# Optimization experiments

Measured on AMD Instinct MI355X. Metric: run time of the kernel, lower is better.

Reference implementation:

```python
import jax, jax.numpy as jnp
import numpy as np

# Sizes
N, E = 100000, 3200000
F_NODE, F_EDGE, LD, HID, L = 4, 4, 6, 16, 8
ALPHA = 1.0
EPS = 1e-6


def setup_inputs() -> dict:
    key = jax.random.key(0)
    ks = jax.random.split(key, 8)
    x = jax.random.normal(ks[0], (N, F_NODE), jnp.float32)
    fixed_mask = jax.random.uniform(ks[1], (N,)) < 0.1
    x = x.at[:, -1].set(jnp.where(fixed_mask, jnp.abs(x[:, -1]) + 1.0, 0.0))
    # positive edge attributes (pipe resistance etc.)
    edge_attr = jax.random.uniform(ks[2], (E, F_EDGE), jnp.float32) * 0.9 + 0.1
    edge_index = jax.random.randint(ks[3], (2, E), 0, N, dtype=jnp.int64)
    d_in = 2 * LD + 2 * F_NODE + F_EDGE  # 24: [x_src, x_dst, attr_src, attr_dst, edge_attr]
    s = 0.1
    W1 = jax.random.normal(ks[4], (L, d_in, HID), jnp.float32) * s
    b1 = jnp.zeros((L, HID), jnp.float32)
    W2 = jax.random.normal(ks[5], (L, HID, LD), jnp.float32) * s
    b2 = jnp.zeros((L, LD), jnp.float32)
    Wf = jax.random.normal(ks[6], (LD, 1), jnp.float32) * s
    bf = jnp.zeros((1,), jnp.float32)
    return {"x": x, "edge_attr": edge_attr, "edge_index": edge_index,
            "W1": W1, "b1": b1, "W2": W2, "b2": b2, "Wf": Wf, "bf": bf}


def reference(x, edge_attr, edge_index, W1, b1, W2, b2, Wf, bf):
    src, dst = edge_index[0], edge_index[1]
    # in-degree for mean aggregation
    deg = jax.ops.segment_sum(jnp.ones((E,), jnp.float32), dst, num_segments=N)
    deg = jnp.maximum(deg, 1.0)
    X = jnp.zeros((N, LD), jnp.float32)
    na_src, na_dst = x[src], x[dst]  # static node-attr gathers reused each layer
    for l in range(L):  # num_convs GNNSConv layers
        m_in = jnp.concatenate([X[src], X[dst], na_src, na_dst, edge_attr], axis=-1)  # [E,24]
        h = jax.nn.relu(m_in @ W1[l] + b1[l])         # per-edge MLP hidden [E,16]
        m = h @ W2[l] + b2[l]                          # per-edge message [E,6]
        agg = jax.ops.segment_sum(m, dst, num_segments=N) / deg[:, None]  # mean aggr
        X = (1.0 - ALPHA) * X + ALPHA * agg            # latent update (alpha_update_x)
        X = jax.nn.relu(X)
    P = jax.nn.relu(X @ Wf + bf)                       # [N,1]
    fixed = x[:, -1]
    P_ = jnp.where(fixed != 0, fixed, P.reshape(-1))   # keep known pressures
    # BalanceConv: gas-network flow from squared-pressure drop, k = edge resistance
    dp2 = P_[src] ** 2 - P_[dst] ** 2
    k = edge_attr[:, 0]
    flows = jnp.sign(dp2) * jnp.sqrt(jnp.abs(dp2) / k + EPS)  # [E]
    inj = x[:, 0]  # nodal injection/demand
    balance = (jax.ops.segment_sum(flows, dst, num_segments=N)
               - jax.ops.segment_sum(flows, src, num_segments=N) + inj)
    imbalance = jnp.sqrt(jnp.sum(balance ** 2))
    return P, flows, jnp.stack([imbalance])
```

## Files before the change

kernel.cpp:

```cpp
#include <hip/hip_runtime.h>
#include <math.h>

#define N_NODES 100000
#define N_EDGES 3200000
#define F_NODE 4
#define F_EDGE 4
#define LD 6
#define HID 16
#define NLAYER 8
#define EPSF 1e-6f

#define NPB 64
#define NBK 1563
#define NBIN 196
#define G1 1000
#define CH (N_EDGES / G1)
#define EPT ((CH + 255) / 256)
#define SPLIT 4
#define NSB (NBIN * SPLIT)

__device__ __forceinline__ unsigned f2bf(float a, float b) {
    unsigned ua = __float_as_uint(a);
    ua = (ua + 0x7fffu + ((ua >> 16) & 1u)) >> 16;
    unsigned ub = __float_as_uint(b);
    ub = (ub + 0x7fffu + ((ub >> 16) & 1u)) & 0xffff0000u;
    return ua | ub;
}
__device__ __forceinline__ float bflo(unsigned u) { return __uint_as_float(u << 16); }
__device__ __forceinline__ float bfhi(unsigned u) { return __uint_as_float(u & 0xffff0000u); }

__global__ __launch_bounds__(256) void hist_kernel(const int* __restrict__ ei,
                                                   int* __restrict__ ghd,
                                                   int* __restrict__ ghs) {
    __shared__ int hd[NBIN];
    __shared__ int hs[NBIN];
    int t = threadIdx.x, blk = blockIdx.x;
    for (int i = t; i < NBIN; i += 256) { hd[i] = 0; hs[i] = 0; }
    __syncthreads();
    int beg = blk * CH, end = beg + CH;
    for (int e = beg + t; e < end; e += 256) {
        atomicAdd(&hs[ei[e] >> 9], 1);
        atomicAdd(&hd[ei[N_EDGES + e] >> 9], 1);
    }
    __syncthreads();
    for (int i = t; i < NBIN; i += 256) {
        ghd[(size_t)i * G1 + blk] = hd[i];
        ghs[(size_t)i * G1 + blk] = hs[i];
    }
}

__global__ __launch_bounds__(256) void scanb_kernel(int* __restrict__ ghd, int* __restrict__ ghs,
                                                    int* __restrict__ totd, int* __restrict__ tots) {
    __shared__ int part[256];
    int b = blockIdx.x, t = threadIdx.x;
#pragma unroll
    for (int a = 0; a < 2; a++) {
        int* g = a ? ghs : ghd;
        int vals[4];
        int sum = 0;
#pragma unroll
        for (int k = 0; k < 4; k++) {
            int idx = t * 4 + k;
            vals[k] = (idx < G1) ? g[(size_t)b * G1 + idx] : 0;
            sum += vals[k];
        }
        part[t] = sum;
        __syncthreads();
        for (int off = 1; off < 256; off <<= 1) {
            int v = (t >= off) ? part[t - off] : 0;
            __syncthreads();
            part[t] += v;
            __syncthreads();
        }
        int excl = part[t] - sum;
#pragma unroll
        for (int k = 0; k < 4; k++) {
            int idx = t * 4 + k;
            if (idx < G1) g[(size_t)b * G1 + idx] = excl;
            excl += vals[k];
        }
        if (t == 0) (a ? tots : totd)[b] = part[255];
        __syncthreads();
    }
}

__global__ __launch_bounds__(256) void totscan_kernel(const int* __restrict__ totd,
                                                      const int* __restrict__ tots,
                                                      int* __restrict__ binbased,
                                                      int* __restrict__ binbases) {
    __shared__ int part[256];
    int t = threadIdx.x;
#pragma unroll
    for (int a = 0; a < 2; a++) {
        const int* tot = a ? tots : totd;
        int* base = a ? binbases : binbased;
        int v = (t < NBIN) ? tot[t] : 0;
        part[t] = v;
        __syncthreads();
        for (int off = 1; off < 256; off <<= 1) {
            int u = (t >= off) ? part[t - off] : 0;
            __syncthreads();
            part[t] += u;
            __syncthreads();
        }
        if (t < NBIN) base[t] = part[t] - v;
        if (t == 0) base[NBIN] = N_EDGES;
        __syncthreads();
    }
}

__global__ __launch_bounds__(256) void scatterA_kernel(const int* __restrict__ ei,
                                                       const float* __restrict__ ea,
                                                       const int* __restrict__ ghd,
                                                       const int* __restrict__ ghs,
                                                       const int* __restrict__ binbased,
                                                       const int* __restrict__ binbases,
                                                       unsigned* __restrict__ aw0,
                                                       unsigned* __restrict__ aw1,
                                                       unsigned* __restrict__ aw2,
                                                       unsigned* __restrict__ sbufA) {
    __shared__ int hcnt[NBIN];
    __shared__ int cdl[NBIN];
    __shared__ int gb[NBIN];
    __shared__ int part[256];
    __shared__ unsigned st0[CH];
    __shared__ unsigned st1[CH];
    __shared__ unsigned st2[CH];
    __shared__ unsigned stg[CH];
    int t = threadIdx.x, blk = blockIdx.x;
    int beg = blk * CH;
    int lidx[EPT];

    for (int i = t; i < NBIN; i += 256) hcnt[i] = 0;
    __syncthreads();
    {
        int k = 0;
        for (int i = t; i < CH; i += 256, k++)
            lidx[k] = atomicAdd(&hcnt[ei[N_EDGES + beg + i] >> 9], 1);
    }
    __syncthreads();
    {
        int own = (t < NBIN) ? hcnt[t] : 0;
        part[t] = own;
        __syncthreads();
        for (int off = 1; off < 256; off <<= 1) {
            int v = (t >= off) ? part[t - off] : 0;
            __syncthreads();
            part[t] += v;
            __syncthreads();
        }
        if (t < NBIN) {
            cdl[t] = part[t] - own;
            gb[t] = binbased[t] + ghd[(size_t)t * G1 + blk];
        }
    }
    __syncthreads();
    {
        int k = 0;
        for (int i = t; i < CH; i += 256, k++) {
            int e = beg + i;
            int s = ei[e];
            int d = ei[N_EDGES + e];
            float4 ev = reinterpret_cast<const float4*>(ea)[e];
            int bin = d >> 9;
            int pos = cdl[bin] + lidx[k];
            st0[pos] = (unsigned)s | ((unsigned)(d & 511) << 17);
            st1[pos] = f2bf(ev.x, ev.y);
            st2[pos] = f2bf(ev.z, ev.w);
            stg[pos] = (unsigned)(gb[bin] + lidx[k]);
        }
    }
    __syncthreads();
    for (int i = t; i < CH; i += 256) {
        unsigned g = stg[i];
        aw0[g] = st0[i];
        aw1[g] = st1[i];
        aw2[g] = st2[i];
    }
    __syncthreads();

    for (int i = t; i < NBIN; i += 256) hcnt[i] = 0;
    __syncthreads();
    {
        int k = 0;
        for (int i = t; i < CH; i += 256, k++)
            lidx[k] = atomicAdd(&hcnt[ei[beg + i] >> 9], 1);
    }
    __syncthreads();
    {
        int own = (t < NBIN) ? hcnt[t] : 0;
        part[t] = own;
        __syncthreads();
        for (int off = 1; off < 256; off <<= 1) {
            int v = (t >= off) ? part[t - off] : 0;
            __syncthreads();
            part[t] += v;
            __syncthreads();
        }
        if (t < NBIN) {
            cdl[t] = part[t] - own;
            gb[t] = binbases[t] + ghs[(size_t)t * G1 + blk];
        }
    }
    __syncthreads();
    {
        int k = 0;
        for (int i = t; i < CH; i += 256, k++) {
            int e = beg + i;
            int s = ei[e];
            int bin = s >> 9;
            int pos = cdl[bin] + lidx[k];
            st0[pos] = (unsigned)e | ((unsigned)(s & 511) << 22);
            stg[pos] = (unsigned)(gb[bin] + lidx[k]);
        }
    }
    __syncthreads();
    for (int i = t; i < CH; i += 256)
        sbufA[stg[i]] = st0[i];
}

__global__ __launch_bounds__(256) void sr_hist(const unsigned* __restrict__ aw0,
                                               const int* __restrict__ binbased,
                                               int* __restrict__ srh) {
    __shared__ int hist[512];
    int bs = blockIdx.x, t = threadIdx.x;
    int b = bs >> 2, h = bs & 3;
    hist[t] = 0; hist[t + 256] = 0;
    __syncthreads();
    int beg = binbased[b], end = binbased[b + 1];
    int len = end - beg;
    int p0 = beg + (int)((long long)len * h / SPLIT);
    int p1 = beg + (int)((long long)len * (h + 1) / SPLIT);
    for (int i = p0 + t; i < p1; i += 256)
        atomicAdd(&hist[(aw0[i] >> 17) & 511u], 1);
    __syncthreads();
    int* g = srh + (size_t)bs * 512;
    g[t] = hist[t];
    g[t + 256] = hist[t + 256];
}

__global__ __launch_bounds__(256) void sr_scat(const unsigned* __restrict__ aw0,
                                               const unsigned* __restrict__ aw1,
                                               const unsigned* __restrict__ aw2,
                                               const int* __restrict__ binbased,
                                               const int* __restrict__ srh,
                                               unsigned* __restrict__ bw0,
                                               unsigned* __restrict__ bw1,
                                               unsigned* __restrict__ bw2,
                                               float* __restrict__ degInv,
                                               int* __restrict__ based_bk) {
    __shared__ int cur[512];
    __shared__ int part[256];
    int bs = blockIdx.x, t = threadIdx.x;
    int b = bs >> 2, h = bs & 3;
    int beg = binbased[b], end = binbased[b + 1];
    int j0 = 2 * t, j1 = 2 * t + 1;
    int tot0 = 0, tot1 = 0, own0 = 0, own1 = 0;
    const int* gb = srh + (size_t)(b << 2) * 512;
#pragma unroll
    for (int hh = 0; hh < SPLIT; hh++) {
        int v0 = gb[hh * 512 + j0];
        int v1 = gb[hh * 512 + j1];
        if (hh < h) { own0 += v0; own1 += v1; }
        tot0 += v0; tot1 += v1;
    }
    int tsum = tot0 + tot1;
    part[t] = tsum;
    __syncthreads();
    for (int off = 1; off < 256; off <<= 1) {
        int v = (t >= off) ? part[t - off] : 0;
        __syncthreads();
        part[t] += v;
        __syncthreads();
    }
    int excl = part[t] - tsum;
    cur[j0] = beg + excl + own0;
    cur[j1] = beg + excl + tot0 + own1;
    if (h == 0) {
        int node0 = b << 9;
        if (node0 + j0 < N_NODES) degInv[node0 + j0] = 1.0f / fmaxf((float)tot0, 1.0f);
        if (node0 + j1 < N_NODES) degInv[node0 + j1] = 1.0f / fmaxf((float)tot1, 1.0f);
        if ((t & 31) == 0) {
            int k = t >> 5;
            int node = node0 + (k << 6);
            if (node < N_NODES) based_bk[(b << 3) + k] = beg + excl;
        }
        if (b == NBIN - 1 && t == 0) based_bk[NBK] = N_EDGES;
    }
    __syncthreads();
    int len = end - beg;
    int p0 = beg + (int)((long long)len * h / SPLIT);
    int p1 = beg + (int)((long long)len * (h + 1) / SPLIT);
    for (int i = p0 + t; i < p1; i += 256) {
        unsigned r0 = aw0[i];
        int nib = (int)((r0 >> 17) & 511u);
        int p = atomicAdd(&cur[nib], 1);
        bw0[p] = (r0 & 0x1FFFFu) | ((unsigned)(nib & 63) << 17);
        bw1[p] = aw1[i];
        bw2[p] = aw2[i];
    }
}

__global__ __launch_bounds__(256) void ss_hist(const unsigned* __restrict__ sbufA,
                                               const int* __restrict__ binbases,
                                               int* __restrict__ ssh) {
    __shared__ int hist[512];
    int bs = blockIdx.x, t = threadIdx.x;
    int b = bs >> 2, h = bs & 3;
    hist[t] = 0; hist[t + 256] = 0;
    __syncthreads();
    int beg = binbases[b], end = binbases[b + 1];
    int len = end - beg;
    int p0 = beg + (int)((long long)len * h / SPLIT);
    int p1 = beg + (int)((long long)len * (h + 1) / SPLIT);
    for (int i = p0 + t; i < p1; i += 256)
        atomicAdd(&hist[(sbufA[i] >> 22) & 511u], 1);
    __syncthreads();
    int* g = ssh + (size_t)bs * 512;
    g[t] = hist[t];
    g[t + 256] = hist[t + 256];
}

__global__ __launch_bounds__(256) void ss_scat(const unsigned* __restrict__ sbufA,
                                               const int* __restrict__ binbases,
                                               const int* __restrict__ ssh,
                                               unsigned* __restrict__ sbufB,
                                               int* __restrict__ bases_bk) {
    __shared__ int cur[512];
    __shared__ int part[256];
    int bs = blockIdx.x, t = threadIdx.x;
    int b = bs >> 2, h = bs & 3;
    int beg = binbases[b], end = binbases[b + 1];
    int j0 = 2 * t, j1 = 2 * t + 1;
    int tot0 = 0, tot1 = 0, own0 = 0, own1 = 0;
    const int* gb = ssh + (size_t)(b << 2) * 512;
#pragma unroll
    for (int hh = 0; hh < SPLIT; hh++) {
        int v0 = gb[hh * 512 + j0];
        int v1 = gb[hh * 512 + j1];
        if (hh < h) { own0 += v0; own1 += v1; }
        tot0 += v0; tot1 += v1;
    }
    int tsum = tot0 + tot1;
    part[t] = tsum;
    __syncthreads();
    for (int off = 1; off < 256; off <<= 1) {
        int v = (t >= off) ? part[t - off] : 0;
        __syncthreads();
        part[t] += v;
        __syncthreads();
    }
    int excl = part[t] - tsum;
    cur[j0] = beg + excl + own0;
    cur[j1] = beg + excl + tot0 + own1;
    if (h == 0) {
        if ((t & 31) == 0) {
            int k = t >> 5;
            int node = (b << 9) + (k << 6);
            if (node < N_NODES) bases_bk[(b << 3) + k] = beg + excl;
        }
        if (b == NBIN - 1 && t == 0) bases_bk[NBK] = N_EDGES;
    }
    __syncthreads();
    int len = end - beg;
    int p0 = beg + (int)((long long)len * h / SPLIT);
    int p1 = beg + (int)((long long)len * (h + 1) / SPLIT);
    for (int i = p0 + t; i < p1; i += 256) {
        unsigned w = sbufA[i];
        int nib = (int)((w >> 22) & 511u);
        int p = atomicAdd(&cur[nib], 1);
        sbufB[p] = (w & 0x3FFFFFu) | ((unsigned)(nib & 63) << 22);
    }
}

__global__ __launch_bounds__(256) void ab_init(const float* __restrict__ x,
                                               const float* __restrict__ W1,
                                               const float* __restrict__ b1,
                                               unsigned* __restrict__ A,
                                               unsigned* __restrict__ B) {
    __shared__ float sW[8 * HID];
    __shared__ float sb[HID];
    int t = threadIdx.x;
    for (int i = t; i < 8 * HID; i += 256) sW[i] = W1[12 * HID + i];
    if (t < HID) sb[t] = b1[t];
    __syncthreads();
    int i = blockIdx.x * 256 + t;
    if (i >= N_NODES) return;
    float4 xv = reinterpret_cast<const float4*>(x)[i];
    float xf[4] = {xv.x, xv.y, xv.z, xv.w};
    float a[HID], bb[HID];
#pragma unroll
    for (int j = 0; j < HID; j++) { a[j] = sb[j]; bb[j] = 0.0f; }
#pragma unroll
    for (int r = 0; r < 4; r++) {
        float v = xf[r];
#pragma unroll
        for (int j = 0; j < HID; j++) {
            a[j]  = fmaf(v, sW[r * HID + j], a[j]);
            bb[j] = fmaf(v, sW[(4 + r) * HID + j], bb[j]);
        }
    }
    uint4* Ao = reinterpret_cast<uint4*>(A + (size_t)i * 8);
    Ao[0] = make_uint4(f2bf(a[0], a[1]), f2bf(a[2], a[3]), f2bf(a[4], a[5]), f2bf(a[6], a[7]));
    Ao[1] = make_uint4(f2bf(a[8], a[9]), f2bf(a[10], a[11]), f2bf(a[12], a[13]), f2bf(a[14], a[15]));
    uint4* Bo = reinterpret_cast<uint4*>(B + (size_t)i * 8);
    Bo[0] = make_uint4(f2bf(bb[0], bb[1]), f2bf(bb[2], bb[3]), f2bf(bb[4], bb[5]), f2bf(bb[6], bb[7]));
    Bo[1] = make_uint4(f2bf(bb[8], bb[9]), f2bf(bb[10], bb[11]), f2bf(bb[12], bb[13]), f2bf(bb[14], bb[15]));
}

template <int LAST>
__global__ __launch_bounds__(512) void edge_layer(const unsigned* __restrict__ bw0,
                                                  const unsigned* __restrict__ bw1,
                                                  const unsigned* __restrict__ bw2,
                                                  const unsigned* __restrict__ Ain,
                                                  const unsigned* __restrict__ Bin,
                                                  const float* __restrict__ x,
                                                  const float* __restrict__ degInv,
                                                  const float* __restrict__ W1l,
                                                  const float* __restrict__ W2l,
                                                  const float* __restrict__ b2l,
                                                  const float* __restrict__ W1n,
                                                  const float* __restrict__ b1n,
                                                  const float* __restrict__ Wf,
                                                  const float* __restrict__ bfp,
                                                  const int* __restrict__ based_bk,
                                                  unsigned* __restrict__ Aout,
                                                  unsigned* __restrict__ Bout,
                                                  float* __restrict__ Pout,
                                                  float* __restrict__ Pbuf) {
    __shared__ float sWea[4 * HID];
    __shared__ float sW2[HID * LD];
    __shared__ float sb2[LD];
    __shared__ float sW1n[20 * HID];
    __shared__ float sb1n[HID];
    __shared__ float sWf[LD];
    __shared__ float sbf;
    __shared__ float accf[LD * NPB];
    __shared__ unsigned sB[NPB * 8];
    int t = threadIdx.x;
    int b = blockIdx.x;
    for (int i = t; i < 4 * HID; i += 512) sWea[i] = W1l[20 * HID + i];
    for (int i = t; i < HID * LD; i += 512) sW2[i] = W2l[i];
    if (t < LD) sb2[t] = b2l[t];
    if (!LAST) {
        for (int i = t; i < 20 * HID; i += 512) sW1n[i] = W1n[i];
        if (t < HID) sb1n[t] = b1n[t];
    } else {
        if (t < LD) sWf[t] = Wf[t];
        if (t == 0) sbf = bfp[0];
    }
    for (int i = t; i < LD * NPB; i += 512) accf[i] = 0.0f;
    {
        size_t base8 = (size_t)(b << 6) * 8;
        for (int i = t; i < NPB * 8; i += 512) {
            size_t gi = base8 + i;
            sB[i] = (gi < (size_t)N_NODES * 8) ? Bin[gi] : 0u;
        }
    }
    __syncthreads();

    int beg = based_bk[b], end = based_bk[b + 1];
    int lane = t & 63;

    for (int base = beg; base < end; base += 512) {
        int p = base + t;
        bool valid = p < end;
        int key = -1;
        float out[LD];
#pragma unroll
        for (int o = 0; o < LD; o++) out[o] = 0.0f;

        if (valid) {
            unsigned r0 = bw0[p];
            unsigned w1 = bw1[p];
            unsigned w2 = bw2[p];
            int s = (int)(r0 & 0x1FFFFu);
            key = (int)((r0 >> 17) & 63u);
            const uint4* Ap = reinterpret_cast<const uint4*>(Ain + (size_t)s * 8);
            uint4 ax = Ap[0], ay = Ap[1];
            const uint4* Bp = reinterpret_cast<const uint4*>(sB) + key * 2;
            uint4 bx = Bp[0], by = Bp[1];
            float h[HID];
            h[0]  = bflo(ax.x) + bflo(bx.x);  h[1]  = bfhi(ax.x) + bfhi(bx.x);
            h[2]  = bflo(ax.y) + bflo(bx.y);  h[3]  = bfhi(ax.y) + bfhi(bx.y);
            h[4]  = bflo(ax.z) + bflo(bx.z);  h[5]  = bfhi(ax.z) + bfhi(bx.z);
            h[6]  = bflo(ax.w) + bflo(bx.w);  h[7]  = bfhi(ax.w) + bfhi(bx.w);
            h[8]  = bflo(ay.x) + bflo(by.x);  h[9]  = bfhi(ay.x) + bfhi(by.x);
            h[10] = bflo(ay.y) + bflo(by.y);  h[11] = bfhi(ay.y) + bfhi(by.y);
            h[12] = bflo(ay.z) + bflo(by.z);  h[13] = bfhi(ay.z) + bfhi(by.z);
            h[14] = bflo(ay.w) + bflo(by.w);  h[15] = bfhi(ay.w) + bfhi(by.w);
            float ef[4] = {bflo(w1), bfhi(w1), bflo(w2), bfhi(w2)};
#pragma unroll
            for (int rr = 0; rr < 4; rr++) {
                float v = ef[rr];
#pragma unroll
                for (int j = 0; j < HID; j++) h[j] = fmaf(v, sWea[rr * HID + j], h[j]);
            }
#pragma unroll
            for (int j = 0; j < HID; j++) h[j] = fmaxf(h[j], 0.0f);
#pragma unroll
            for (int o = 0; o < LD; o++) out[o] = sb2[o];
#pragma unroll
            for (int j = 0; j < HID; j++) {
                float hj = h[j];
#pragma unroll
                for (int o = 0; o < LD; o++) out[o] = fmaf(hj, sW2[j * LD + o], out[o]);
            }
        }

#pragma unroll
        for (int st = 1; st < 64; st <<= 1) {
            int kup = __shfl_up(key, st, 64);
            bool same = (lane >= st) && (kup == key);
#pragma unroll
            for (int o = 0; o < LD; o++) {
                float v = __shfl_up(out[o], st, 64);
                if (same) out[o] += v;
            }
        }
        int knx = __shfl_down(key, 1, 64);
        bool tail = (lane == 63) || (knx != key);
        if (valid && tail) {
#pragma unroll
            for (int o = 0; o < LD; o++) atomicAdd(&accf[o * NPB + key], out[o]);
        }
    }
    __syncthreads();

    if (t < NPB) {
        int gid = (b << 6) + t;
        if (gid < N_NODES) {
            float inv = degInv[gid];
            float Xv[LD];
#pragma unroll
            for (int o = 0; o < LD; o++) Xv[o] = fmaxf(accf[o * NPB + t] * inv, 0.0f);
            if (LAST) {
                float a2 = sbf;
#pragma unroll
                for (int o = 0; o < LD; o++) a2 = fmaf(Xv[o], sWf[o], a2);
                float P = fmaxf(a2, 0.0f);
                Pout[gid] = P;
                float fx = x[gid * F_NODE + 3];
                Pbuf[gid] = (fx != 0.0f) ? fx : P;
            } else {
                float4 xv = reinterpret_cast<const float4*>(x)[gid];
                float xf[4] = {xv.x, xv.y, xv.z, xv.w};
                float a[HID], bb[HID];
#pragma unroll
                for (int j = 0; j < HID; j++) { a[j] = sb1n[j]; bb[j] = 0.0f; }
#pragma unroll
                for (int rr = 0; rr < LD; rr++) {
                    float v = Xv[rr];
#pragma unroll
                    for (int j = 0; j < HID; j++) {
                        a[j]  = fmaf(v, sW1n[rr * HID + j], a[j]);
                        bb[j] = fmaf(v, sW1n[(LD + rr) * HID + j], bb[j]);
                    }
                }
#pragma unroll
                for (int rr = 0; rr < 4; rr++) {
                    float v = xf[rr];
#pragma unroll
                    for (int j = 0; j < HID; j++) {
                        a[j]  = fmaf(v, sW1n[(12 + rr) * HID + j], a[j]);
                        bb[j] = fmaf(v, sW1n[(16 + rr) * HID + j], bb[j]);
                    }
                }
                uint4* Ao = reinterpret_cast<uint4*>(Aout + (size_t)gid * 8);
                Ao[0] = make_uint4(f2bf(a[0], a[1]), f2bf(a[2], a[3]), f2bf(a[4], a[5]), f2bf(a[6], a[7]));
                Ao[1] = make_uint4(f2bf(a[8], a[9]), f2bf(a[10], a[11]), f2bf(a[12], a[13]), f2bf(a[14], a[15]));
                uint4* Bo = reinterpret_cast<uint4*>(Bout + (size_t)gid * 8);
                Bo[0] = make_uint4(f2bf(bb[0], bb[1]), f2bf(bb[2], bb[3]), f2bf(bb[4], bb[5]), f2bf(bb[6], bb[7]));
                Bo[1] = make_uint4(f2bf(bb[8], bb[9]), f2bf(bb[10], bb[11]), f2bf(bb[12], bb[13]), f2bf(bb[14], bb[15]));
            }
        }
    }
}

__global__ __launch_bounds__(256) void flows_noatomic(const int* __restrict__ ei,
                                                      const float* __restrict__ ea,
                                                      const float* __restrict__ Pbuf,
                                                      float* __restrict__ flows_out) {
    int e = blockIdx.x * 256 + threadIdx.x;
    if (e >= N_EDGES) return;
    int s = ei[e];
    int d = ei[N_EDGES + e];
    float ps = Pbuf[s], pd = Pbuf[d];
    float dp2 = ps * ps - pd * pd;
    float k = ea[(size_t)e * F_EDGE];
    float sg = (dp2 > 0.0f) ? 1.0f : ((dp2 < 0.0f) ? -1.0f : 0.0f);
    flows_out[e] = sg * sqrtf(fabsf(dp2) / k + EPSF);
}

__global__ __launch_bounds__(256) void balance_in(const unsigned* __restrict__ bw0,
                                                  const unsigned* __restrict__ bw1,
                                                  const float* __restrict__ Pbuf,
                                                  const float* __restrict__ x,
                                                  const int* __restrict__ based_bk,
                                                  float* __restrict__ bal) {
    __shared__ float acc[NPB];
    __shared__ float pdl[NPB];
    int t = threadIdx.x;
    int b = blockIdx.x;
    if (t < NPB) {
        acc[t] = 0.0f;
        int gid = (b << 6) + t;
        pdl[t] = (gid < N_NODES) ? Pbuf[gid] : 0.0f;
    }
    __syncthreads();
    int beg = based_bk[b], end = based_bk[b + 1];
    int lane = t & 63;
    for (int base = beg; base < end; base += 256) {
        int p = base + t;
        bool valid = p < end;
        int key = -1;
        float f = 0.0f;
        if (valid) {
            unsigned r0 = bw0[p];
            int s = (int)(r0 & 0x1FFFFu);
            key = (int)((r0 >> 17) & 63u);
            float ps = Pbuf[s];
            float pd = pdl[key];
            float k = bflo(bw1[p]);
            float dp2 = ps * ps - pd * pd;
            float sg = (dp2 > 0.0f) ? 1.0f : ((dp2 < 0.0f) ? -1.0f : 0.0f);
            f = sg * sqrtf(fabsf(dp2) / k + EPSF);
        }
#pragma unroll
        for (int st = 1; st < 64; st <<= 1) {
            int kup = __shfl_up(key, st, 64);
            float v = __shfl_up(f, st, 64);
            if ((lane >= st) && (kup == key)) f += v;
        }
        int knx = __shfl_down(key, 1, 64);
        bool tail = (lane == 63) || (knx != key);
        if (valid && tail) atomicAdd(&acc[key], f);
    }
    __syncthreads();
    if (t < NPB) {
        int gid = (b << 6) + t;
        if (gid < N_NODES) bal[gid] = acc[t] + x[gid * F_NODE + 0];
    }
}

__global__ __launch_bounds__(256) void balance_out(const unsigned* __restrict__ sbufB,
                                                   const float* __restrict__ flows,
                                                   const int* __restrict__ bases_bk,
                                                   const float* __restrict__ bal,
                                                   float* __restrict__ imb2) {
    __shared__ float acc[NPB];
    int t = threadIdx.x;
    if (t < NPB) acc[t] = 0.0f;
    __syncthreads();
    int b = blockIdx.x;
    int beg = bases_bk[b], end = bases_bk[b + 1];
    int lane = t & 63;
    for (int base = beg; base < end; base += 256) {
        int q = base + t;
        bool valid = q < end;
        int key = -1;
        float f = 0.0f;
        if (valid) {
            unsigned u = sbufB[q];
            key = (int)((u >> 22) & 63u);
            f = flows[u & 0x3FFFFFu];
        }
#pragma unroll
        for (int st = 1; st < 64; st <<= 1) {
            int kup = __shfl_up(key, st, 64);
            float v = __shfl_up(f, st, 64);
            if ((lane >= st) && (kup == key)) f += v;
        }
        int knx = __shfl_down(key, 1, 64);
        bool tail = (lane == 63) || (knx != key);
        if (valid && tail) atomicAdd(&acc[key], f);
    }
    __syncthreads();
    if (t < NPB) {
        float v = 0.0f;
        int gid = (b << 6) + t;
        if (gid < N_NODES) {
            float bv = bal[gid] - acc[t];
            v = bv * bv;
        }
#pragma unroll
        for (int off = 32; off > 0; off >>= 1) v += __shfl_down(v, off, 64);
        if (t == 0) atomicAdd(imb2, v);
    }
}

__global__ void fin_kernel(const float* __restrict__ imb2, float* __restrict__ out) {
    out[0] = sqrtf(imb2[0]);
}

extern "C" void kernel_launch(void* const* d_in, const int* in_sizes, int n_in,
                              void* d_out, int out_size, void* d_ws, size_t ws_size,
                              hipStream_t stream) {
    const float* x   = (const float*)d_in[0];
    const float* ea  = (const float*)d_in[1];
    const int*   ei  = (const int*)d_in[2];
    const float* W1  = (const float*)d_in[3];
    const float* b1  = (const float*)d_in[4];
    const float* W2  = (const float*)d_in[5];
    const float* b2  = (const float*)d_in[6];
    const float* Wf  = (const float*)d_in[7];
    const float* bf_ = (const float*)d_in[8];
    float* out = (float*)d_out;

    const size_t N = N_NODES, E = N_EDGES;

    size_t o = 0;
    auto alloc = [&](size_t n) { size_t r = o; o += (n + 3) & ~(size_t)3; return r; };
    size_t o_bw0      = alloc(E);
    size_t o_bw1      = alloc(E);
    size_t o_bw2      = alloc(E);
    size_t o_aw0      = alloc(E);
    size_t o_aw1      = alloc(E);
    size_t o_aw2      = alloc(E);
    size_t o_sbufA    = alloc(E);
    size_t o_ghd      = alloc((size_t)NBIN * G1);
    size_t o_ghs      = alloc((size_t)NBIN * G1);
    size_t o_srh      = alloc((size_t)NSB * 512);
    size_t o_ssh      = alloc((size_t)NSB * 512);
    size_t o_totd     = alloc(NBIN);
    size_t o_tots     = alloc(NBIN);
    size_t o_binbased = alloc(NBIN + 1);
    size_t o_binbases = alloc(NBIN + 1);
    size_t o_basedbk  = alloc(NBK + 1);
    size_t o_basesbk  = alloc(NBK + 1);
    size_t o_degInv   = alloc(N);
    size_t o_A0       = alloc(8 * N);
    size_t o_B0       = alloc(8 * N);
    size_t o_A1       = alloc(8 * N);
    size_t o_B1       = alloc(8 * N);
    size_t o_Pbuf     = alloc(N);
    size_t o_bal      = alloc(N);
    size_t o_imb2     = alloc(16);
    (void)o;

    int* wsi = (int*)d_ws;
    unsigned* bw0      = (unsigned*)(wsi + o_bw0);
    unsigned* bw1      = (unsigned*)(wsi + o_bw1);
    unsigned* bw2      = (unsigned*)(wsi + o_bw2);
    unsigned* aw0      = (unsigned*)(wsi + o_aw0);
    unsigned* aw1      = (unsigned*)(wsi + o_aw1);
    unsigned* aw2      = (unsigned*)(wsi + o_aw2);
    unsigned* sbufA    = (unsigned*)(wsi + o_sbufA);
    unsigned* sbufB    = (unsigned*)(wsi + o_aw0);
    int*      ghd      = wsi + o_ghd;
    int*      ghs      = wsi + o_ghs;
    int*      srh      = wsi + o_srh;
    int*      ssh      = wsi + o_ssh;
    int*      totd     = wsi + o_totd;
    int*      tots     = wsi + o_tots;
    int*      binbased = wsi + o_binbased;
    int*      binbases = wsi + o_binbases;
    int*      based_bk = wsi + o_basedbk;
    int*      bases_bk = wsi + o_basesbk;
    float*    degInv   = (float*)(wsi + o_degInv);
    unsigned* A0       = (unsigned*)(wsi + o_A0);
    unsigned* B0       = (unsigned*)(wsi + o_B0);
    unsigned* A1       = (unsigned*)(wsi + o_A1);
    unsigned* B1       = (unsigned*)(wsi + o_B1);
    float*    Pbuf     = (float*)(wsi + o_Pbuf);
    float*    bal      = (float*)(wsi + o_bal);
    float*    imb2     = (float*)(wsi + o_imb2);

    const int NB = (N_NODES + 255) / 256;
    const int EB = (N_EDGES + 255) / 256;

    hipMemsetAsync(imb2, 0, sizeof(float), stream);

    hist_kernel<<<G1, 256, 0, stream>>>(ei, ghd, ghs);
    scanb_kernel<<<NBIN, 256, 0, stream>>>(ghd, ghs, totd, tots);
    totscan_kernel<<<1, 256, 0, stream>>>(totd, tots, binbased, binbases);
    scatterA_kernel<<<G1, 256, 0, stream>>>(ei, ea, ghd, ghs, binbased, binbases,
                                            aw0, aw1, aw2, sbufA);
    sr_hist<<<NSB, 256, 0, stream>>>(aw0, binbased, srh);
    sr_scat<<<NSB, 256, 0, stream>>>(aw0, aw1, aw2, binbased, srh,
                                     bw0, bw1, bw2, degInv, based_bk);
    ss_hist<<<NSB, 256, 0, stream>>>(sbufA, binbases, ssh);
    ss_scat<<<NSB, 256, 0, stream>>>(sbufA, binbases, ssh, sbufB, bases_bk);

    ab_init<<<NB, 256, 0, stream>>>(x, W1, b1, A0, B0);

    for (int l = 0; l < NLAYER; l++) {
        const unsigned* Ain = (l & 1) ? A1 : A0;
        const unsigned* Bin = (l & 1) ? B1 : B0;
        unsigned* Aout = (l & 1) ? A0 : A1;
        unsigned* Bout = (l & 1) ? B0 : B1;
        const float* W1l = W1 + (size_t)l * 24 * HID;
        const float* W2l = W2 + (size_t)l * HID * LD;
        const float* b2l = b2 + (size_t)l * LD;
        if (l < NLAYER - 1) {
            edge_layer<0><<<NBK, 512, 0, stream>>>(bw0, bw1, bw2, Ain, Bin, x, degInv,
                                                   W1l, W2l, b2l,
                                                   W1 + (size_t)(l + 1) * 24 * HID,
                                                   b1 + (size_t)(l + 1) * HID,
                                                   Wf, bf_, based_bk,
                                                   Aout, Bout, out, Pbuf);
        } else {
            edge_layer<1><<<NBK, 512, 0, stream>>>(bw0, bw1, bw2, Ain, Bin, x, degInv,
                                                   W1l, W2l, b2l,
                                                   W1, b1, Wf, bf_, based_bk,
                                                   Aout, Bout, out, Pbuf);
        }
    }

    flows_noatomic<<<EB, 256, 0, stream>>>(ei, ea, Pbuf, out + N);
    balance_in<<<NBK, 256, 0, stream>>>(bw0, bw1, Pbuf, x, based_bk, bal);
    balance_out<<<NBK, 256, 0, stream>>>(sbufB, out + N, bases_bk, bal, imb2);
    fin_kernel<<<1, 1, 0, stream>>>(imb2, out + (size_t)N + E);
}
```

Measured before the change: 960.0 us.

## Process four sorted edges per thread and make scatter sub-blocks own key ranges

Measured after the change: 2.140 ms. 123% more time.

```diff
diff --git a/kernel.cpp b/kernel.cpp
--- a/kernel.cpp
+++ b/kernel.cpp
@@ -255,14 +255,12 @@
     int b = bs >> 2, h = bs & 3;
     int beg = binbased[b], end = binbased[b + 1];
     int j0 = 2 * t, j1 = 2 * t + 1;
-    int tot0 = 0, tot1 = 0, own0 = 0, own1 = 0;
+    int tot0 = 0, tot1 = 0;
     const int* gb = srh + (size_t)(b << 2) * 512;
 #pragma unroll
     for (int hh = 0; hh < SPLIT; hh++) {
-        int v0 = gb[hh * 512 + j0];
-        int v1 = gb[hh * 512 + j1];
-        if (hh < h) { own0 += v0; own1 += v1; }
-        tot0 += v0; tot1 += v1;
+        tot0 += gb[hh * 512 + j0];
+        tot1 += gb[hh * 512 + j1];
     }
     int tsum = tot0 + tot1;
     part[t] = tsum;
@@ -274,8 +272,8 @@
         __syncthreads();
     }
     int excl = part[t] - tsum;
-    cur[j0] = beg + excl + own0;
-    cur[j1] = beg + excl + tot0 + own1;
+    cur[j0] = beg + excl;
+    cur[j1] = beg + excl + tot0;
     if (h == 0) {
         int node0 = b << 9;
         if (node0 + j0 < N_NODES) degInv[node0 + j0] = 1.0f / fmaxf((float)tot0, 1.0f);
@@ -288,16 +286,16 @@
         if (b == NBIN - 1 && t == 0) based_bk[NBK] = N_EDGES;
     }
     __syncthreads();
-    int len = end - beg;
-    int p0 = beg + (int)((long long)len * h / SPLIT);
-    int p1 = beg + (int)((long long)len * (h + 1) / SPLIT);
-    for (int i = p0 + t; i < p1; i += 256) {
+    int lo = h << 7, hi = lo + 128;
+    for (int i = beg + t; i < end; i += 256) {
         unsigned r0 = aw0[i];
         int nib = (int)((r0 >> 17) & 511u);
-        int p = atomicAdd(&cur[nib], 1);
-        bw0[p] = (r0 & 0x1FFFFu) | ((unsigned)(nib & 63) << 17);
-        bw1[p] = aw1[i];
-        bw2[p] = aw2[i];
+        if (nib >= lo && nib < hi) {
+            int p = atomicAdd(&cur[nib], 1);
+            bw0[p] = (r0 & 0x1FFFFu) | ((unsigned)(nib & 63) << 17);
+            bw1[p] = aw1[i];
+            bw2[p] = aw2[i];
+        }
     }
 }
 
@@ -332,14 +330,12 @@
     int b = bs >> 2, h = bs & 3;
     int beg = binbases[b], end = binbases[b + 1];
     int j0 = 2 * t, j1 = 2 * t + 1;
-    int tot0 = 0, tot1 = 0, own0 = 0, own1 = 0;
+    int tot0 = 0, tot1 = 0;
     const int* gb = ssh + (size_t)(b << 2) * 512;
 #pragma unroll
     for (int hh = 0; hh < SPLIT; hh++) {
-        int v0 = gb[hh * 512 + j0];
-        int v1 = gb[hh * 512 + j1];
-        if (hh < h) { own0 += v0; own1 += v1; }
-        tot0 += v0; tot1 += v1;
+        tot0 += gb[hh * 512 + j0];
+        tot1 += gb[hh * 512 + j1];
     }
     int tsum = tot0 + tot1;
     part[t] = tsum;
@@ -351,8 +347,8 @@
         __syncthreads();
     }
     int excl = part[t] - tsum;
-    cur[j0] = beg + excl + own0;
-    cur[j1] = beg + excl + tot0 + own1;
+    cur[j0] = beg + excl;
+    cur[j1] = beg + excl + tot0;
     if (h == 0) {
         if ((t & 31) == 0) {
             int k = t >> 5;
@@ -362,14 +358,14 @@
         if (b == NBIN - 1 && t == 0) bases_bk[NBK] = N_EDGES;
     }
     __syncthreads();
-    int len = end - beg;
-    int p0 = beg + (int)((long long)len * h / SPLIT);
-    int p1 = beg + (int)((long long)len * (h + 1) / SPLIT);
-    for (int i = p0 + t; i < p1; i += 256) {
+    int lo = h << 7, hi = lo + 128;
+    for (int i = beg + t; i < end; i += 256) {
         unsigned w = sbufA[i];
         int nib = (int)((w >> 22) & 511u);
-        int p = atomicAdd(&cur[nib], 1);
-        sbufB[p] = (w & 0x3FFFFFu) | ((unsigned)(nib & 63) << 22);
+        if (nib >= lo && nib < hi) {
+            int p = atomicAdd(&cur[nib], 1);
+            sbufB[p] = (w & 0x3FFFFFu) | ((unsigned)(nib & 63) << 22);
+        }
     }
 }
 
@@ -435,7 +431,7 @@
     __shared__ float sb1n[HID];
     __shared__ float sWf[LD];
     __shared__ float sbf;
-    __shared__ float accf[LD * NPB];
+    __shared__ float accf[NPB * 8];
     __shared__ unsigned sB[NPB * 8];
     int t = threadIdx.x;
     int b = blockIdx.x;
@@ -449,7 +445,7 @@
         if (t < LD) sWf[t] = Wf[t];
         if (t == 0) sbf = bfp[0];
     }
-    for (int i = t; i < LD * NPB; i += 512) accf[i] = 0.0f;
+    if (t < NPB * 8) accf[t] = 0.0f;
     {
         size_t base8 = (size_t)(b << 6) * 8;
         for (int i = t; i < NPB * 8; i += 512) {
@@ -460,51 +456,80 @@
     __syncthreads();
 
     int beg = based_bk[b], end = based_bk[b + 1];
+    int abeg = beg & ~3;
+    int nchunk = (end - abeg + 3) >> 2;
     int lane = t & 63;
 
-    for (int base = beg; base < end; base += 512) {
-        int p = base + t;
-        bool valid = p < end;
+    for (int cb = 0; cb < nchunk; cb += 512) {
+        int c = cb + t;
         int key = -1;
-        float out[LD];
-#pragma unroll
-        for (int o = 0; o < LD; o++) out[o] = 0.0f;
-
-        if (valid) {
-            unsigned r0 = bw0[p];
-            unsigned w1 = bw1[p];
-            unsigned w2 = bw2[p];
-            int s = (int)(r0 & 0x1FFFFu);
-            key = (int)((r0 >> 17) & 63u);
-            const uint4* Ap = reinterpret_cast<const uint4*>(Ain + (size_t)s * 8);
-            uint4 ax = Ap[0], ay = Ap[1];
-            const uint4* Bp = reinterpret_cast<const uint4*>(sB) + key * 2;
-            uint4 bx = Bp[0], by = Bp[1];
-            float h[HID];
-            h[0]  = bflo(ax.x) + bflo(bx.x);  h[1]  = bfhi(ax.x) + bfhi(bx.x);
-            h[2]  = bflo(ax.y) + bflo(bx.y);  h[3]  = bfhi(ax.y) + bfhi(bx.y);
-            h[4]  = bflo(ax.z) + bflo(bx.z);  h[5]  = bfhi(ax.z) + bfhi(bx.z);
-            h[6]  = bflo(ax.w) + bflo(bx.w);  h[7]  = bfhi(ax.w) + bfhi(bx.w);
-            h[8]  = bflo(ay.x) + bflo(by.x);  h[9]  = bfhi(ay.x) + bfhi(by.x);
-            h[10] = bflo(ay.y) + bflo(by.y);  h[11] = bfhi(ay.y) + bfhi(by.y);
-            h[12] = bflo(ay.z) + bflo(by.z);  h[13] = bfhi(ay.z) + bfhi(by.z);
-            h[14] = bflo(ay.w) + bflo(by.w);  h[15] = bfhi(ay.w) + bfhi(by.w);
-            float ef[4] = {bflo(w1), bfhi(w1), bflo(w2), bfhi(w2)};
-#pragma unroll
-            for (int rr = 0; rr < 4; rr++) {
-                float v = ef[rr];
-#pragma unroll
-                for (int j = 0; j < HID; j++) h[j] = fmaf(v, sWea[rr * HID + j], h[j]);
+        float sum[LD];
+#pragma unroll
+        for (int o = 0; o < LD; o++) sum[o] = 0.0f;
+
+        if (c < nchunk) {
+            int p0 = abeg + (c << 2);
+            uint4 r0 = *reinterpret_cast<const uint4*>(bw0 + p0);
+            uint4 r1 = *reinterpret_cast<const uint4*>(bw1 + p0);
+            uint4 r2 = *reinterpret_cast<const uint4*>(bw2 + p0);
+            unsigned w0a[4] = {r0.x, r0.y, r0.z, r0.w};
+            unsigned w1a[4] = {r1.x, r1.y, r1.z, r1.w};
+            unsigned w2a[4] = {r2.x, r2.y, r2.z, r2.w};
+            uint4 axr[4], ayr[4];
+#pragma unroll
+            for (int j = 0; j < 4; j++) {
+                int s = (int)(w0a[j] & 0x1FFFFu);
+                const uint4* Ap = reinterpret_cast<const uint4*>(Ain + (size_t)s * 8);
+                axr[j] = Ap[0];
+                ayr[j] = Ap[1];
             }
 #pragma unroll
-            for (int j = 0; j < HID; j++) h[j] = fmaxf(h[j], 0.0f);
-#pragma unroll
-            for (int o = 0; o < LD; o++) out[o] = sb2[o];
-#pragma unroll
-            for (int j = 0; j < HID; j++) {
-                float hj = h[j];
-#pragma unroll
-                for (int o = 0; o < LD; o++) out[o] = fmaf(hj, sW2[j * LD + o], out[o]);
+            for (int j = 0; j < 4; j++) {
+                int p = p0 + j;
+                if (p < beg || p >= end) continue;
+                int k2 = (int)((w0a[j] >> 17) & 63u);
+                if (k2 != key) {
+                    if (key >= 0) {
+#pragma unroll
+                        for (int o = 0; o < LD; o++)
+                            atomicAdd(&accf[(key << 3) + o], sum[o]);
+                    }
+                    key = k2;
+#pragma unroll
+                    for (int o = 0; o < LD; o++) sum[o] = 0.0f;
+                }
+                const uint4* Bp = reinterpret_cast<const uint4*>(sB) + (k2 << 1);
+                uint4 bx = Bp[0], by = Bp[1];
+                uint4 ax = axr[j], ay = ayr[j];
+                float h[HID];
+                h[0]  = bflo(ax.x) + bflo(bx.x);  h[1]  = bfhi(ax.x) + bfhi(bx.x);
+                h[2]  = bflo(ax.y) + bflo(bx.y);  h[3]  = bfhi(ax.y) + bfhi(bx.y);
+                h[4]  = bflo(ax.z) + bflo(bx.z);  h[5]  = bfhi(ax.z) + bfhi(bx.z);
+                h[6]  = bflo(ax.w) + bflo(bx.w);  h[7]  = bfhi(ax.w) + bfhi(bx.w);
+                h[8]  = bflo(ay.x) + bflo(by.x);  h[9]  = bfhi(ay.x) + bfhi(by.x);
+                h[10] = bflo(ay.y) + bflo(by.y);  h[11] = bfhi(ay.y) + bfhi(by.y);
+                h[12] = bflo(ay.z) + bflo(by.z);  h[13] = bfhi(ay.z) + bfhi(by.z);
+                h[14] = bflo(ay.w) + bflo(by.w);  h[15] = bfhi(ay.w) + bfhi(by.w);
+                float ef[4] = {bflo(w1a[j]), bfhi(w1a[j]), bflo(w2a[j]), bfhi(w2a[j])};
+#pragma unroll
+                for (int rr = 0; rr < 4; rr++) {
+                    float v = ef[rr];
+#pragma unroll
+                    for (int jj = 0; jj < HID; jj++) h[jj] = fmaf(v, sWea[rr * HID + jj], h[jj]);
+                }
+#pragma unroll
+                for (int jj = 0; jj < HID; jj++) h[jj] = fmaxf(h[jj], 0.0f);
+                float mo[LD];
+#pragma unroll
+                for (int o = 0; o < LD; o++) mo[o] = sb2[o];
+#pragma unroll
+                for (int jj = 0; jj < HID; jj++) {
+                    float hj = h[jj];
+#pragma unroll
+                    for (int o = 0; o < LD; o++) mo[o] = fmaf(hj, sW2[jj * LD + o], mo[o]);
+                }
+#pragma unroll
+                for (int o = 0; o < LD; o++) sum[o] += mo[o];
             }
         }
 
@@ -514,15 +539,16 @@
             bool same = (lane >= st) && (kup == key);
 #pragma unroll
             for (int o = 0; o < LD; o++) {
-                float v = __shfl_up(out[o], st, 64);
-                if (same) out[o] += v;
+                float v = __shfl_up(sum[o], st, 64);
+                if (same) sum[o] += v;
             }
         }
         int knx = __shfl_down(key, 1, 64);
         bool tail = (lane == 63) || (knx != key);
-        if (valid && tail) {
-#pragma unroll
-            for (int o = 0; o < LD; o++) atomicAdd(&accf[o * NPB + key], out[o]);
+        if (tail && key >= 0) {
+#pragma unroll
+            for (int o = 0; o < LD; o++)
+                atomicAdd(&accf[(key << 3) + o], sum[o]);
         }
     }
     __syncthreads();
@@ -533,7 +559,7 @@
             float inv = degInv[gid];
             float Xv[LD];
 #pragma unroll
-            for (int o = 0; o < LD; o++) Xv[o] = fmaxf(accf[o * NPB + t] * inv, 0.0f);
+            for (int o = 0; o < LD; o++) Xv[o] = fmaxf(accf[(t << 3) + o] * inv, 0.0f);
             if (LAST) {
                 float a2 = sbf;
 #pragma unroll
```

## Partition radix scatter by destination sub-bucket range and transpose accumulator layout

Applied to the files above, without the earlier changes.

New measurement: 949.9 us. No clear change (-1.1%).

```diff
diff --git a/kernel.cpp b/kernel.cpp
--- a/kernel.cpp
+++ b/kernel.cpp
@@ -255,14 +255,12 @@
     int b = bs >> 2, h = bs & 3;
     int beg = binbased[b], end = binbased[b + 1];
     int j0 = 2 * t, j1 = 2 * t + 1;
-    int tot0 = 0, tot1 = 0, own0 = 0, own1 = 0;
+    int tot0 = 0, tot1 = 0;
     const int* gb = srh + (size_t)(b << 2) * 512;
 #pragma unroll
     for (int hh = 0; hh < SPLIT; hh++) {
-        int v0 = gb[hh * 512 + j0];
-        int v1 = gb[hh * 512 + j1];
-        if (hh < h) { own0 += v0; own1 += v1; }
-        tot0 += v0; tot1 += v1;
+        tot0 += gb[hh * 512 + j0];
+        tot1 += gb[hh * 512 + j1];
     }
     int tsum = tot0 + tot1;
     part[t] = tsum;
@@ -274,8 +272,8 @@
         __syncthreads();
     }
     int excl = part[t] - tsum;
-    cur[j0] = beg + excl + own0;
-    cur[j1] = beg + excl + tot0 + own1;
+    cur[j0] = beg + excl;
+    cur[j1] = beg + excl + tot0;
     if (h == 0) {
         int node0 = b << 9;
         if (node0 + j0 < N_NODES) degInv[node0 + j0] = 1.0f / fmaxf((float)tot0, 1.0f);
@@ -288,16 +286,16 @@
         if (b == NBIN - 1 && t == 0) based_bk[NBK] = N_EDGES;
     }
     __syncthreads();
-    int len = end - beg;
-    int p0 = beg + (int)((long long)len * h / SPLIT);
-    int p1 = beg + (int)((long long)len * (h + 1) / SPLIT);
-    for (int i = p0 + t; i < p1; i += 256) {
+    int lo = h << 7, hi = lo + 128;
+    for (int i = beg + t; i < end; i += 256) {
         unsigned r0 = aw0[i];
         int nib = (int)((r0 >> 17) & 511u);
-        int p = atomicAdd(&cur[nib], 1);
-        bw0[p] = (r0 & 0x1FFFFu) | ((unsigned)(nib & 63) << 17);
-        bw1[p] = aw1[i];
-        bw2[p] = aw2[i];
+        if (nib >= lo && nib < hi) {
+            int p = atomicAdd(&cur[nib], 1);
+            bw0[p] = (r0 & 0x1FFFFu) | ((unsigned)(nib & 63) << 17);
+            bw1[p] = aw1[i];
+            bw2[p] = aw2[i];
+        }
     }
 }
 
@@ -332,14 +330,12 @@
     int b = bs >> 2, h = bs & 3;
     int beg = binbases[b], end = binbases[b + 1];
     int j0 = 2 * t, j1 = 2 * t + 1;
-    int tot0 = 0, tot1 = 0, own0 = 0, own1 = 0;
+    int tot0 = 0, tot1 = 0;
     const int* gb = ssh + (size_t)(b << 2) * 512;
 #pragma unroll
     for (int hh = 0; hh < SPLIT; hh++) {
-        int v0 = gb[hh * 512 + j0];
-        int v1 = gb[hh * 512 + j1];
-        if (hh < h) { own0 += v0; own1 += v1; }
-        tot0 += v0; tot1 += v1;
+        tot0 += gb[hh * 512 + j0];
+        tot1 += gb[hh * 512 + j1];
     }
     int tsum = tot0 + tot1;
     part[t] = tsum;
@@ -351,8 +347,8 @@
         __syncthreads();
     }
     int excl = part[t] - tsum;
-    cur[j0] = beg + excl + own0;
-    cur[j1] = beg + excl + tot0 + own1;
+    cur[j0] = beg + excl;
+    cur[j1] = beg + excl + tot0;
     if (h == 0) {
         if ((t & 31) == 0) {
             int k = t >> 5;
@@ -362,14 +358,14 @@
         if (b == NBIN - 1 && t == 0) bases_bk[NBK] = N_EDGES;
     }
     __syncthreads();
-    int len = end - beg;
-    int p0 = beg + (int)((long long)len * h / SPLIT);
-    int p1 = beg + (int)((long long)len * (h + 1) / SPLIT);
-    for (int i = p0 + t; i < p1; i += 256) {
+    int lo = h << 7, hi = lo + 128;
+    for (int i = beg + t; i < end; i += 256) {
         unsigned w = sbufA[i];
         int nib = (int)((w >> 22) & 511u);
-        int p = atomicAdd(&cur[nib], 1);
-        sbufB[p] = (w & 0x3FFFFFu) | ((unsigned)(nib & 63) << 22);
+        if (nib >= lo && nib < hi) {
+            int p = atomicAdd(&cur[nib], 1);
+            sbufB[p] = (w & 0x3FFFFFu) | ((unsigned)(nib & 63) << 22);
+        }
     }
 }
 
@@ -435,7 +431,7 @@
     __shared__ float sb1n[HID];
     __shared__ float sWf[LD];
     __shared__ float sbf;
-    __shared__ float accf[LD * NPB];
+    __shared__ float accf[NPB * 8];
     __shared__ unsigned sB[NPB * 8];
     int t = threadIdx.x;
     int b = blockIdx.x;
@@ -449,7 +445,7 @@
         if (t < LD) sWf[t] = Wf[t];
         if (t == 0) sbf = bfp[0];
     }
-    for (int i = t; i < LD * NPB; i += 512) accf[i] = 0.0f;
+    if (t < NPB * 8) accf[t] = 0.0f;
     {
         size_t base8 = (size_t)(b << 6) * 8;
         for (int i = t; i < NPB * 8; i += 512) {
@@ -478,7 +474,7 @@
             key = (int)((r0 >> 17) & 63u);
             const uint4* Ap = reinterpret_cast<const uint4*>(Ain + (size_t)s * 8);
             uint4 ax = Ap[0], ay = Ap[1];
-            const uint4* Bp = reinterpret_cast<const uint4*>(sB) + key * 2;
+            const uint4* Bp = reinterpret_cast<const uint4*>(sB) + (key << 1);
             uint4 bx = Bp[0], by = Bp[1];
             float h[HID];
             h[0]  = bflo(ax.x) + bflo(bx.x);  h[1]  = bfhi(ax.x) + bfhi(bx.x);
@@ -522,7 +518,7 @@
         bool tail = (lane == 63) || (knx != key);
         if (valid && tail) {
 #pragma unroll
-            for (int o = 0; o < LD; o++) atomicAdd(&accf[o * NPB + key], out[o]);
+            for (int o = 0; o < LD; o++) atomicAdd(&accf[(key << 3) + o], out[o]);
         }
     }
     __syncthreads();
@@ -533,7 +529,7 @@
             float inv = degInv[gid];
             float Xv[LD];
 #pragma unroll
-            for (int o = 0; o < LD; o++) Xv[o] = fmaxf(accf[o * NPB + t] * inv, 0.0f);
+            for (int o = 0; o < LD; o++) Xv[o] = fmaxf(accf[(t << 3) + o] * inv, 0.0f);
             if (LAST) {
                 float a2 = sbf;
 #pragma unroll
```
